# Kernel tuning notes

Hardware: AMD Instinct MI355X
Metric: run time of the kernel (lower is better)

## Reference

```python
import jax, jax.numpy as jnp
import numpy as np
from jax import lax

B, L, DM = 1, 2048, 1024   # batch, seq len, d_model
N = 16                     # d_state
K = 4                      # d_conv
DI = 2 * DM                # d_inner = d_model * expand_factor


def silu(v):
    return v * jax.nn.sigmoid(v)


def setup_inputs() -> dict:
    key = jax.random.key(0)
    ks = jax.random.split(key, 11)
    s = 0.02
    f32 = jnp.float32
    return {
        "x": jax.random.normal(ks[0], (B, L, DM), f32),
        "W_in": jax.random.normal(ks[1], (2 * DI, DM), f32) * s,
        "b_in": jnp.zeros((2 * DI,), f32),
        "W_conv": jax.random.normal(ks[2], (DI, 1, K), f32) * s,  # depthwise conv kernel (torch layout)
        "b_conv": jnp.zeros((DI,), f32),
        "W_x": jax.random.normal(ks[3], (DI + 2 * N, DI), f32) * s,
        "b_x": jnp.zeros((DI + 2 * N,), f32),
        "W_out": jax.random.normal(ks[4], (DM, DI), f32) * s,
        "b_out": jnp.zeros((DM,), f32),
        "A_log": jax.random.normal(ks[5], (DI, N), f32),
        "D": jnp.ones((DI,), f32),
    }


def reference(x, W_in, b_in, W_conv, b_conv, W_x, b_x, W_out, b_out, A_log, D):
    Bsz = x.shape[0]
    # in_proj and split into ssm branch / residual gate branch
    xr = x @ W_in.T + b_in                      # (B, L, 2*DI)
    xi, res = jnp.split(xr, 2, axis=-1)
    # causal depthwise conv1d: torch pads (K-1) both sides then slices [:L] == left-pad K-1
    xc = jnp.transpose(xi, (0, 2, 1))           # (B, DI, L)
    xc = lax.conv_general_dilated(
        xc, W_conv, window_strides=(1,), padding=[(K - 1, 0)],
        dimension_numbers=("NCH", "OIH", "NCH"), feature_group_count=DI,
    ) + b_conv[None, :, None]
    xi = silu(jnp.transpose(xc, (0, 2, 1)))     # (B, L, DI)
    # selective-scan parameterization
    proj = xi @ W_x.T + b_x                      # (B, L, DI + 2N)
    delta = jax.nn.softplus(proj[..., :DI])      # (B, L, DI)
    B_ssm = proj[..., DI:DI + N]                 # (B, L, N)
    C_ssm = proj[..., DI + N:]                   # (B, L, N)
    A = -jnp.exp(A_log)                          # (DI, N)
    dA = jnp.exp(delta[..., None] * A)                               # (B, L, DI, N)
    dBx = delta[..., None] * B_ssm[:, :, None, :] * xi[..., None]    # (B, L, DI, N)

    def step(h, inp):
        da, dbx, c = inp
        h = da * h + dbx                         # (B, DI, N)
        y = jnp.einsum("bdn,bn->bd", h, c)
        return h, y

    h0 = jnp.zeros((Bsz, DI, N), x.dtype)
    _, ys = lax.scan(
        step, h0,
        (jnp.swapaxes(dA, 0, 1), jnp.swapaxes(dBx, 0, 1), jnp.swapaxes(C_ssm, 0, 1)),
    )
    y = jnp.swapaxes(ys, 0, 1) + xi * D          # skip connection
    y = y * silu(res)                            # gate
    return y @ W_out.T + b_out                   # (B, L, DM)
```

## Files before the change

### kernel.cpp

```cpp
#include <hip/hip_runtime.h>
#include <stdint.h>

#define L_SEQ 2048
#define DMODEL 1024
#define DI_DIM 2048
#define NSSM 16
#define NPROJ 2080
#define NCHUNK 64
#define LCHUNK 32

typedef __attribute__((ext_vector_type(8))) short bf16x8;
typedef __attribute__((ext_vector_type(4))) float f32x4;

__device__ __forceinline__ float bf2f(unsigned short u) {
  union { uint32_t u; float f; } v; v.u = (uint32_t)u << 16; return v.f;
}
__device__ __forceinline__ unsigned short f2bf(float f) {
  union { float f; uint32_t u; } v; v.f = f;
  uint32_t u = v.u;
  return (unsigned short)((u + 0x7fffu + ((u >> 16) & 1u)) >> 16);
}
__device__ __forceinline__ void async16(const void* g, void* l) {
  __builtin_amdgcn_global_load_lds(
      (__attribute__((address_space(1))) void*)(g),
      (__attribute__((address_space(3))) void*)(l), 16, 0, 0);
}
__device__ __forceinline__ float softplusf(float p) {
  return (p > 20.f) ? p : __logf(1.f + __expf(p));
}
__device__ __forceinline__ float siluf(float x) {
  return x * __builtin_amdgcn_rcpf(1.f + __expf(-x));
}

#define CVT_N1 524288
#define CVT_N2 (CVT_N1 + 1048576)
#define CVT_N3 (CVT_N2 + 1064960)
__global__ void k_convert3(const float* __restrict__ x, const float* __restrict__ win,
                           const float* __restrict__ wx, unsigned short* __restrict__ xb,
                           unsigned short* __restrict__ winb, unsigned short* __restrict__ wxb) {
  int i = blockIdx.x * 256 + threadIdx.x;
  const float4* src; unsigned short* dst; int j;
  if (i < CVT_N1)      { src = (const float4*)x;   dst = xb;   j = i; }
  else if (i < CVT_N2) { src = (const float4*)win; dst = winb; j = i - CVT_N1; }
  else if (i < CVT_N3) { src = (const float4*)wx;  dst = wxb;  j = i - CVT_N2; }
  else return;
  float4 v = src[j];
  ushort4 o;
  o.x = f2bf(v.x); o.y = f2bf(v.y); o.z = f2bf(v.z); o.w = f2bf(v.w);
  ((ushort4*)dst)[j] = o;
}

__global__ void k_f32_to_bf16(const float* __restrict__ in,
                              unsigned short* __restrict__ out, int n4) {
  int i = blockIdx.x * blockDim.x + threadIdx.x;
  if (i < n4) {
    const float4 v = ((const float4*)in)[i];
    ushort4 o;
    o.x = f2bf(v.x); o.y = f2bf(v.y); o.z = f2bf(v.z); o.w = f2bf(v.w);
    ((ushort4*)out)[i] = o;
  }
}

template <typename OutT, int KB>
__global__ __launch_bounds__(256) void k_gemm_bt(
    const unsigned short* __restrict__ A, const unsigned short* __restrict__ B,
    const float* __restrict__ bias, OutT* __restrict__ C,
    int M, int N, int K) {
  constexpr int NH = KB / 32;
  __shared__ unsigned short As[2][NH][64 * 32];
  __shared__ unsigned short Bs[2][NH][128 * 32];
  const int tid = threadIdx.x;
  const int wave = tid >> 6;
  const int lane = tid & 63;
  const int m0 = blockIdx.y * 64;
  const int n0 = blockIdx.x * 128;
  const int kLen = K / gridDim.z;
  const int kLo = blockIdx.z * kLen;

  const int srow = lane >> 2;
  const int scol = ((lane & 3) ^ ((lane >> 3) & 3)) * 8;
  int ar = m0 + wave * 16 + srow;         if (ar > M - 1) ar = M - 1;
  int br0 = n0 + wave * 32 + srow;        if (br0 > N - 1) br0 = N - 1;
  int br1 = n0 + wave * 32 + 16 + srow;   if (br1 > N - 1) br1 = N - 1;
  const unsigned short* ap  = A + (size_t)ar * K + scol + kLo;
  const unsigned short* bp0 = B + (size_t)br0 * K + scol + kLo;
  const unsigned short* bp1 = B + (size_t)br1 * K + scol + kLo;
  const int soA  = wave * 512;
  const int soB0 = (wave * 2) * 512;
  const int soB1 = (wave * 2 + 1) * 512;

  const int mrow = lane & 15;
  const int swz8 = (((lane >> 4) ^ ((mrow >> 1) & 3)) * 8);
  const int ro = mrow * 32 + swz8;

  f32x4 acc[4][2];
#pragma unroll
  for (int i = 0; i < 4; i++)
#pragma unroll
    for (int j = 0; j < 2; j++) acc[i][j] = (f32x4){0.f, 0.f, 0.f, 0.f};

  const int niter = kLen / KB;

#define STAGE(BUF, KT)                                                         \
  {                                                                            \
    _Pragma("unroll")                                                          \
    for (int hh = 0; hh < NH; hh++) {                                          \
      async16(ap + (KT) + hh * 32, &As[BUF][hh][soA]);                         \
      async16(bp0 + (KT) + hh * 32, &Bs[BUF][hh][soB0]);                       \
      async16(bp1 + (KT) + hh * 32, &Bs[BUF][hh][soB1]);                       \
    }                                                                          \
  }

#define GEMM_COMPUTE(BUF)                                                      \
  {                                                                            \
    _Pragma("unroll")                                                          \
    for (int hh = 0; hh < NH; hh++) {                                          \
      bf16x8 af[4], bfv[2];                                                    \
      _Pragma("unroll")                                                        \
      for (int i = 0; i < 4; i++)                                              \
        af[i] = *(const bf16x8*)&As[BUF][hh][i * 512 + ro];                    \
      _Pragma("unroll")                                                        \
      for (int j = 0; j < 2; j++)                                              \
        bfv[j] = *(const bf16x8*)&Bs[BUF][hh][(wave * 2 + j) * 512 + ro];      \
      _Pragma("unroll")                                                        \
      for (int i = 0; i < 4; i++)                                              \
        _Pragma("unroll")                                                      \
        for (int j = 0; j < 2; j++)                                            \
          acc[i][j] = __builtin_amdgcn_mfma_f32_16x16x32_bf16(af[i], bfv[j],   \
                                                          acc[i][j], 0, 0, 0); \
    }                                                                          \
  }

  STAGE(0, 0)

  for (int it = 0; it < niter; it += 2) {
    __syncthreads();
    STAGE(1, (it + 1) * KB)
    GEMM_COMPUTE(0)
    __syncthreads();
    if (it + 2 < niter) STAGE(0, (it + 2) * KB)
    GEMM_COMPUTE(1)
  }
#undef STAGE
#undef GEMM_COMPUTE

  const bool withBias = (gridDim.z == 1);
  OutT* Cz = C + (size_t)blockIdx.z * ((size_t)M * N);
#pragma unroll
  for (int j = 0; j < 2; j++) {
    int col = n0 + wave * 32 + j * 16 + (lane & 15);
    if (col < N) {
      float bv = withBias ? bias[col] : 0.f;
#pragma unroll
      for (int i = 0; i < 4; i++) {
        int rbase = m0 + i * 16 + (lane >> 4) * 4;
#pragma unroll
        for (int r = 0; r < 4; r++) {
          float v = acc[i][j][r] + bv;
          if constexpr (sizeof(OutT) == 2)
            Cz[(size_t)(rbase + r) * N + col] = (OutT)f2bf(v);
          else
            Cz[(size_t)(rbase + r) * N + col] = (OutT)v;
        }
      }
    }
  }
}

__global__ void k_reduce_out(const float* __restrict__ part, const float* __restrict__ bias,
                             float* __restrict__ out) {
  int i = blockIdx.x * 256 + threadIdx.x;
  float4 a = ((const float4*)part)[i];
  float4 b = ((const float4*)(part + (size_t)L_SEQ * DMODEL))[i];
  int col = (i * 4) & (DMODEL - 1);
  float4 bb = *(const float4*)&bias[col];
  float4 o;
  o.x = a.x + b.x + bb.x; o.y = a.y + b.y + bb.y;
  o.z = a.z + b.z + bb.z; o.w = a.w + b.w + bb.w;
  ((float4*)out)[i] = o;
}

__global__ void k_conv_silu(const unsigned short* __restrict__ xr,
                            const float* __restrict__ Wc,
                            const float* __restrict__ bc,
                            unsigned short* __restrict__ xcb) {
  int idx = blockIdx.x * blockDim.x + threadIdx.x;
  if (idx >= L_SEQ * DI_DIM) return;
  int t = idx >> 11;
  int d = idx & (DI_DIM - 1);
  float acc = bc[d];
  const float* wd = Wc + d * 4;
  if (t >= 3) acc += bf2f(xr[(size_t)(t - 3) * (2 * DI_DIM) + d]) * wd[0];
  if (t >= 2) acc += bf2f(xr[(size_t)(t - 2) * (2 * DI_DIM) + d]) * wd[1];
  if (t >= 1) acc += bf2f(xr[(size_t)(t - 1) * (2 * DI_DIM) + d]) * wd[2];
  acc += bf2f(xr[(size_t)t * (2 * DI_DIM) + d]) * wd[3];
  xcb[idx] = f2bf(siluf(acc));
}

__global__ __launch_bounds__(256) void k_scan_a(
    const float* __restrict__ proj, const unsigned short* __restrict__ xcb,
    const float* __restrict__ A_log,
    float* __restrict__ Sdelta, float* __restrict__ hstate) {
  __shared__ float Bsh[LCHUNK * NSSM];
  const int d = blockIdx.x * 256 + threadIdx.x;
  const int c = blockIdx.y;
  const int t0 = c * LCHUNK;
  for (int i = threadIdx.x; i < LCHUNK * NSSM; i += 256) {
    int t = i >> 4, n = i & 15;
    Bsh[i] = proj[(size_t)(t0 + t) * NPROJ + DI_DIM + n];
  }
  __syncthreads();
  float Ar[NSSM], h[NSSM];
#pragma unroll
  for (int n = 0; n < NSSM; n++) {
    Ar[n] = -__expf(A_log[d * NSSM + n]);
    h[n] = 0.f;
  }
  const float* pp = proj + (size_t)t0 * NPROJ + d;
  const unsigned short* xp = xcb + (size_t)t0 * DI_DIM + d;
  float p_nxt = pp[0];
  unsigned short x_nxt = xp[0];
  float sd = 0.f;
  for (int t = 0; t < LCHUNK; t++) {
    float p = p_nxt;
    unsigned short xu = x_nxt;
    if (t + 1 < LCHUNK) {
      p_nxt = pp[(size_t)(t + 1) * NPROJ];
      x_nxt = xp[(size_t)(t + 1) * DI_DIM];
    }
    float delta = softplusf(p);
    float dx = delta * bf2f(xu);
    sd += delta;
#pragma unroll
    for (int n = 0; n < NSSM; n++)
      h[n] = __expf(delta * Ar[n]) * h[n] + dx * Bsh[t * NSSM + n];
  }
  Sdelta[(size_t)c * DI_DIM + d] = sd;
#pragma unroll
  for (int n = 0; n < NSSM; n++)
    hstate[((size_t)c * DI_DIM + d) * NSSM + n] = h[n];
}

__global__ void k_scan_b(const float* __restrict__ A_log,
                         const float* __restrict__ Sdelta,
                         float* __restrict__ hstate) {
  int tid = blockIdx.x * 256 + threadIdx.x;
  int d = tid >> 4;
  float A = -__expf(A_log[tid]);
  float carry = 0.f;
  float v_nxt = hstate[tid];
  float s_nxt = Sdelta[d];
  for (int c = 0; c < NCHUNK; c++) {
    float v = v_nxt, s = s_nxt;
    if (c + 1 < NCHUNK) {
      v_nxt = hstate[(size_t)(c + 1) * DI_DIM * NSSM + tid];
      s_nxt = Sdelta[(size_t)(c + 1) * DI_DIM + d];
    }
    hstate[(size_t)c * DI_DIM * NSSM + tid] = carry;
    carry = __expf(A * s) * carry + v;
  }
}

__global__ __launch_bounds__(256) void k_scan_c(
    const float* __restrict__ proj, const unsigned short* __restrict__ xcb,
    const float* __restrict__ A_log, const float* __restrict__ h0,
    const float* __restrict__ Dvec, const unsigned short* __restrict__ xr,
    unsigned short* __restrict__ ybf) {
  __shared__ float Bsh[LCHUNK * NSSM];
  __shared__ float Csh[LCHUNK * NSSM];
  const int d = blockIdx.x * 256 + threadIdx.x;
  const int c = blockIdx.y;
  const int t0 = c * LCHUNK;
  for (int i = threadIdx.x; i < LCHUNK * NSSM; i += 256) {
    int t = i >> 4, n = i & 15;
    Bsh[i] = proj[(size_t)(t0 + t) * NPROJ + DI_DIM + n];
    Csh[i] = proj[(size_t)(t0 + t) * NPROJ + DI_DIM + NSSM + n];
  }
  __syncthreads();
  float Ar[NSSM], h[NSSM];
#pragma unroll
  for (int n = 0; n < NSSM; n++) {
    Ar[n] = -__expf(A_log[d * NSSM + n]);
    h[n] = h0[((size_t)c * DI_DIM + d) * NSSM + n];
  }
  float Dd = Dvec[d];
  const float* pp = proj + (size_t)t0 * NPROJ + d;
  const unsigned short* xp = xcb + (size_t)t0 * DI_DIM + d;
  const unsigned short* rp = xr + (size_t)t0 * (2 * DI_DIM) + DI_DIM + d;
  float p_nxt = pp[0];
  unsigned short x_nxt = xp[0];
  unsigned short r_nxt = rp[0];
  for (int t = 0; t < LCHUNK; t++) {
    float p = p_nxt;
    unsigned short xu = x_nxt, ru = r_nxt;
    if (t + 1 < LCHUNK) {
      p_nxt = pp[(size_t)(t + 1) * NPROJ];
      x_nxt = xp[(size_t)(t + 1) * DI_DIM];
      r_nxt = rp[(size_t)(t + 1) * (2 * DI_DIM)];
    }
    float delta = softplusf(p);
    float xi = bf2f(xu);
    float dx = delta * xi;
    float y = 0.f;
#pragma unroll
    for (int n = 0; n < NSSM; n++) {
      h[n] = __expf(delta * Ar[n]) * h[n] + dx * Bsh[t * NSSM + n];
      y += h[n] * Csh[t * NSSM + n];
    }
    y += xi * Dd;
    y *= siluf(bf2f(ru));
    ybf[(size_t)(t0 + t) * DI_DIM + d] = f2bf(y);
  }
}

extern "C" void kernel_launch(void* const* d_in, const int* in_sizes, int n_in,
                              void* d_out, int out_size, void* d_ws, size_t ws_size,
                              hipStream_t stream) {
  const float* x      = (const float*)d_in[0];
  const float* W_in   = (const float*)d_in[1];
  const float* b_in   = (const float*)d_in[2];
  const float* W_conv = (const float*)d_in[3];
  const float* b_conv = (const float*)d_in[4];
  const float* W_x    = (const float*)d_in[5];
  const float* b_x    = (const float*)d_in[6];
  const float* W_out  = (const float*)d_in[7];
  const float* b_out  = (const float*)d_in[8];
  const float* A_log  = (const float*)d_in[9];
  const float* Dv     = (const float*)d_in[10];
  float* out = (float*)d_out;

  char* ws = (char*)d_ws;
  size_t off = 0;
  auto alloc = [&](size_t bytes) { void* p = ws + off; off += (bytes + 255) & ~(size_t)255; return p; };
  unsigned short* win_bf = (unsigned short*)alloc((size_t)4096 * DMODEL * 2);
  unsigned short* wx_bf  = (unsigned short*)alloc((size_t)NPROJ * DI_DIM * 2);
  unsigned short* x_bf   = (unsigned short*)alloc((size_t)L_SEQ * DMODEL * 2);
  unsigned short* xr_bf  = (unsigned short*)alloc((size_t)L_SEQ * 2 * DI_DIM * 2);
  unsigned short* xcb    = (unsigned short*)alloc((size_t)L_SEQ * DI_DIM * 2);
  float* proj            = (float*)alloc((size_t)L_SEQ * NPROJ * 4);
  float* Sdelta          = (float*)alloc((size_t)NCHUNK * DI_DIM * 4);
  float* hstate          = (float*)alloc((size_t)NCHUNK * DI_DIM * NSSM * 4);
  if (off > ws_size) return;
  unsigned short* ybf     = win_bf;
  unsigned short* wout_bf = x_bf;
  float* part             = proj;

  k_convert3<<<CVT_N3 / 256, 256, 0, stream>>>(x, W_in, W_x, x_bf, win_bf, wx_bf);

  {
    dim3 g(4096 / 128, L_SEQ / 64);
    k_gemm_bt<unsigned short, 32><<<g, 256, 0, stream>>>(x_bf, win_bf, b_in, xr_bf, L_SEQ, 4096, DMODEL);
  }
  k_f32_to_bf16<<<(DMODEL * DI_DIM / 4) / 256, 256, 0, stream>>>(W_out, wout_bf, DMODEL * DI_DIM / 4);
  k_conv_silu<<<(L_SEQ * DI_DIM) / 256, 256, 0, stream>>>(xr_bf, W_conv, b_conv, xcb);
  {
    dim3 g((NPROJ + 127) / 128, L_SEQ / 64);
    k_gemm_bt<float, 64><<<g, 256, 0, stream>>>(xcb, wx_bf, b_x, proj, L_SEQ, NPROJ, DI_DIM);
  }
  {
    dim3 ga(DI_DIM / 256, NCHUNK);
    k_scan_a<<<ga, 256, 0, stream>>>(proj, xcb, A_log, Sdelta, hstate);
    k_scan_b<<<(DI_DIM * NSSM) / 256, 256, 0, stream>>>(A_log, Sdelta, hstate);
    k_scan_c<<<ga, 256, 0, stream>>>(proj, xcb, A_log, hstate, Dv, xr_bf, ybf);
  }
  {
    dim3 g(DMODEL / 128, L_SEQ / 64, 2);
    k_gemm_bt<float, 64><<<g, 256, 0, stream>>>(ybf, wout_bf, b_out, part, L_SEQ, DMODEL, DI_DIM);
    k_reduce_out<<<(L_SEQ * DMODEL / 4) / 256, 256, 0, stream>>>(part, b_out, out);
  }
}
```

Measured before the change: 278.4 us.

## Replace double-buffered GEMM with multi-stage vmcnt-gated LDS pipeline

The GEMM's two-buffer, two-barrier-per-iteration loop becomes a ring of 3 or 4 LDS stages, each 32 deep in K. Each iteration waits with explicit s_waitcnt vmcnt so that DEPTH-1 asynchronous global-to-LDS loads stay in flight, then issues one barrier, the next stage's load and the MFMA compute. The goal is to hide more global load latency and cut barriers per unit of K. In exchange the hard-coded vmcnt counts depend on exactly three loads per stage, and the epilogue is unrolled by hand for each depth.

After: 278.1 us. Within noise of the previous version (-0.1%).

```diff
diff --git a/kernel.cpp b/kernel.cpp
--- a/kernel.cpp
+++ b/kernel.cpp
@@ -31,6 +31,13 @@
 __device__ __forceinline__ float siluf(float x) {
   return x * __builtin_amdgcn_rcpf(1.f + __expf(-x));
 }
+
+#define WAITV(N) asm volatile("s_waitcnt vmcnt(" #N ")" ::: "memory")
+#define GBAR()                                   \
+  {                                              \
+    __builtin_amdgcn_s_barrier();                \
+    asm volatile("" ::: "memory");               \
+  }
 
 #define CVT_N1 524288
 #define CVT_N2 (CVT_N1 + 1048576)
@@ -61,14 +68,13 @@
   }
 }
 
-template <typename OutT, int KB>
+template <typename OutT, int DEPTH>
 __global__ __launch_bounds__(256) void k_gemm_bt(
     const unsigned short* __restrict__ A, const unsigned short* __restrict__ B,
     const float* __restrict__ bias, OutT* __restrict__ C,
     int M, int N, int K) {
-  constexpr int NH = KB / 32;
-  __shared__ unsigned short As[2][NH][64 * 32];
-  __shared__ unsigned short Bs[2][NH][128 * 32];
+  __shared__ unsigned short As[DEPTH][64 * 32];
+  __shared__ unsigned short Bs[DEPTH][128 * 32];
   const int tid = threadIdx.x;
   const int wave = tid >> 6;
   const int lane = tid & 63;
@@ -99,47 +105,56 @@
 #pragma unroll
     for (int j = 0; j < 2; j++) acc[i][j] = (f32x4){0.f, 0.f, 0.f, 0.f};
 
-  const int niter = kLen / KB;
+  const int niter = kLen / 32;
 
 #define STAGE(BUF, KT)                                                         \
   {                                                                            \
-    _Pragma("unroll")                                                          \
-    for (int hh = 0; hh < NH; hh++) {                                          \
-      async16(ap + (KT) + hh * 32, &As[BUF][hh][soA]);                         \
-      async16(bp0 + (KT) + hh * 32, &Bs[BUF][hh][soB0]);                       \
-      async16(bp1 + (KT) + hh * 32, &Bs[BUF][hh][soB1]);                       \
-    }                                                                          \
+    async16(ap + (KT), &As[BUF][soA]);                                         \
+    async16(bp0 + (KT), &Bs[BUF][soB0]);                                       \
+    async16(bp1 + (KT), &Bs[BUF][soB1]);                                       \
   }
 
 #define GEMM_COMPUTE(BUF)                                                      \
   {                                                                            \
+    bf16x8 af[4], bfv[2];                                                      \
     _Pragma("unroll")                                                          \
-    for (int hh = 0; hh < NH; hh++) {                                          \
-      bf16x8 af[4], bfv[2];                                                    \
-      _Pragma("unroll")                                                        \
-      for (int i = 0; i < 4; i++)                                              \
-        af[i] = *(const bf16x8*)&As[BUF][hh][i * 512 + ro];                    \
+    for (int i = 0; i < 4; i++)                                                \
+      af[i] = *(const bf16x8*)&As[BUF][i * 512 + ro];                          \
+    _Pragma("unroll")                                                          \
+    for (int j = 0; j < 2; j++)                                                \
+      bfv[j] = *(const bf16x8*)&Bs[BUF][(wave * 2 + j) * 512 + ro];            \
+    _Pragma("unroll")                                                          \
+    for (int i = 0; i < 4; i++)                                                \
       _Pragma("unroll")                                                        \
       for (int j = 0; j < 2; j++)                                              \
-        bfv[j] = *(const bf16x8*)&Bs[BUF][hh][(wave * 2 + j) * 512 + ro];      \
-      _Pragma("unroll")                                                        \
-      for (int i = 0; i < 4; i++)                                              \
-        _Pragma("unroll")                                                      \
-        for (int j = 0; j < 2; j++)                                            \
-          acc[i][j] = __builtin_amdgcn_mfma_f32_16x16x32_bf16(af[i], bfv[j],   \
-                                                          acc[i][j], 0, 0, 0); \
-    }                                                                          \
-  }
-
-  STAGE(0, 0)
-
-  for (int it = 0; it < niter; it += 2) {
-    __syncthreads();
-    STAGE(1, (it + 1) * KB)
-    GEMM_COMPUTE(0)
-    __syncthreads();
-    if (it + 2 < niter) STAGE(0, (it + 2) * KB)
-    GEMM_COMPUTE(1)
+        acc[i][j] = __builtin_amdgcn_mfma_f32_16x16x32_bf16(af[i], bfv[j],     \
+                                                        acc[i][j], 0, 0, 0);   \
+  }
+
+#pragma unroll
+  for (int j = 0; j < DEPTH - 1; j++) STAGE(j, j * 32)
+
+  int cur = 0, nxt = DEPTH - 1;
+  for (int t = 0; t < niter - (DEPTH - 1); t++) {
+    if constexpr (DEPTH == 4) { WAITV(6); } else { WAITV(3); }
+    GBAR()
+    STAGE(nxt, (t + DEPTH - 1) * 32)
+    GEMM_COMPUTE(cur)
+    cur = (cur == DEPTH - 1) ? 0 : cur + 1;
+    nxt = (nxt == DEPTH - 1) ? 0 : nxt + 1;
+  }
+  if constexpr (DEPTH == 4) {
+    WAITV(6); GBAR()
+    GEMM_COMPUTE(cur) cur = (cur == 3) ? 0 : cur + 1;
+    WAITV(3); GBAR()
+    GEMM_COMPUTE(cur) cur = (cur == 3) ? 0 : cur + 1;
+    WAITV(0); GBAR()
+    GEMM_COMPUTE(cur)
+  } else {
+    WAITV(3); GBAR()
+    GEMM_COMPUTE(cur) cur = (cur == DEPTH - 1) ? 0 : cur + 1;
+    WAITV(0); GBAR()
+    GEMM_COMPUTE(cur)
   }
 #undef STAGE
 #undef GEMM_COMPUTE
@@ -349,13 +364,13 @@
 
   {
     dim3 g(4096 / 128, L_SEQ / 64);
-    k_gemm_bt<unsigned short, 32><<<g, 256, 0, stream>>>(x_bf, win_bf, b_in, xr_bf, L_SEQ, 4096, DMODEL);
+    k_gemm_bt<unsigned short, 3><<<g, 256, 0, stream>>>(x_bf, win_bf, b_in, xr_bf, L_SEQ, 4096, DMODEL);
   }
   k_f32_to_bf16<<<(DMODEL * DI_DIM / 4) / 256, 256, 0, stream>>>(W_out, wout_bf, DMODEL * DI_DIM / 4);
   k_conv_silu<<<(L_SEQ * DI_DIM) / 256, 256, 0, stream>>>(xr_bf, W_conv, b_conv, xcb);
   {
     dim3 g((NPROJ + 127) / 128, L_SEQ / 64);
-    k_gemm_bt<float, 64><<<g, 256, 0, stream>>>(xcb, wx_bf, b_x, proj, L_SEQ, NPROJ, DI_DIM);
+    k_gemm_bt<float, 4><<<g, 256, 0, stream>>>(xcb, wx_bf, b_x, proj, L_SEQ, NPROJ, DI_DIM);
   }
   {
     dim3 ga(DI_DIM / 256, NCHUNK);
@@ -365,7 +380,7 @@
   }
   {
     dim3 g(DMODEL / 128, L_SEQ / 64, 2);
-    k_gemm_bt<float, 64><<<g, 256, 0, stream>>>(ybf, wout_bf, b_out, part, L_SEQ, DMODEL, DI_DIM);
+    k_gemm_bt<float, 4><<<g, 256, 0, stream>>>(ybf, wout_bf, b_out, part, L_SEQ, DMODEL, DI_DIM);
     k_reduce_out<<<(L_SEQ * DMODEL / 4) / 256, 256, 0, stream>>>(part, b_out, out);
   }
 }
```
